# Performance work log

Hardware: AMD Instinct MI355X
Metric: run time of the kernel (lower is better)

The kernel has to match this reference:

```python
import jax, jax.numpy as jnp
import numpy as np

B, L, D, E, H = 8, 2048, 1024, 8, 2048


def setup_inputs() -> dict:
    key = jax.random.key(0)
    ks = jax.random.split(key, 5)
    scale_in = 1.0 / np.sqrt(D)
    scale_h = 1.0 / np.sqrt(H)
    return {
        "x": jax.random.normal(ks[0], (B, L, D), dtype=jnp.float32),
        "Wg": jax.random.normal(ks[1], (D, E), dtype=jnp.float32) * scale_in,
        "bg": jnp.zeros((E,), dtype=jnp.float32),
        "W1": jax.random.normal(ks[2], (E, D, H), dtype=jnp.float32) * scale_in,
        "b1": jnp.zeros((E, H), dtype=jnp.float32),
        "W2": jax.random.normal(ks[3], (E, H, D), dtype=jnp.float32) * scale_h,
        "b2": jnp.zeros((E, D), dtype=jnp.float32),
    }


def reference(x, Wg, bg, W1, b1, W2, b2):
    # x: [B, L, D] -> tokens [N, D]
    Bs, Ls, Ds = x.shape
    x_flat = x.reshape(-1, Ds)                                   # [N, D]
    gate_logits = x_flat @ Wg + bg                               # [N, E]
    gate_weights = jax.nn.softmax(gate_logits, axis=-1)          # [N, E]
    # top-1 gate (torch.topk with k=1)
    top_idx = jnp.argmax(gate_weights, axis=-1)                  # [N]
    top_w = jnp.max(gate_weights, axis=-1)                       # [N]
    # dense all-expert compute (matches torch.stack over experts)
    hidden = jax.nn.relu(jnp.einsum('nd,edh->neh', x_flat, W1) + b1)  # [N, E, H]
    expert_outputs = jnp.einsum('neh,ehd->ned', hidden, W2) + b2     # [N, E, D]
    # gather the selected expert per token, scale by its gate weight
    selected = jnp.take_along_axis(expert_outputs, top_idx[:, None, None], axis=1)[:, 0, :]  # [N, D]
    out_flat = top_w[:, None] * selected                          # [N, D]
    out = out_flat.reshape(Bs, Ls, Ds)
    return out, gate_weights
```

## Files before the change

kernel.cpp:

```cpp
#include <hip/hip_runtime.h>
#include <hip/hip_bf16.h>

#define N_TOK 16384
#define D_DIM 1024
#define E_NUM 8
#define H_DIM 2048
#define MT 32
#define FFN_BLK 512

typedef __attribute__((ext_vector_type(8))) short short8;
typedef __attribute__((ext_vector_type(4))) float floatx4;

__device__ __forceinline__ unsigned short f2bf_bits(float f) {
    __hip_bfloat16 h = __float2bfloat16(f);
    return *reinterpret_cast<unsigned short*>(&h);
}

__device__ __forceinline__ void async16(const void* g, void* l) {
    __builtin_amdgcn_global_load_lds(
        (const __attribute__((address_space(1))) unsigned int*)g,
        (__attribute__((address_space(3))) unsigned int*)l,
        16, 0, 0);
}

__global__ __launch_bounds__(256) void moe_gate_kernel(
    const float* __restrict__ x,
    const float* __restrict__ Wg,
    const float* __restrict__ bg,
    float* __restrict__ gw_out,
    float* __restrict__ topw,
    int* __restrict__ topidx,
    unsigned short* __restrict__ xb) {
    int wave = (blockIdx.x * blockDim.x + threadIdx.x) >> 6;
    int lane = threadIdx.x & 63;
    if (wave >= N_TOK) return;
    const float* xr = x + (size_t)wave * D_DIM;

    float4 xv[4];
#pragma unroll
    for (int i = 0; i < 4; i++)
        xv[i] = *(const float4*)(xr + i * 256 + lane * 4);

#pragma unroll
    for (int i = 0; i < 4; i++) {
        ushort4 o;
        o.x = f2bf_bits(xv[i].x); o.y = f2bf_bits(xv[i].y);
        o.z = f2bf_bits(xv[i].z); o.w = f2bf_bits(xv[i].w);
        *(ushort4*)(xb + (size_t)wave * D_DIM + i * 256 + lane * 4) = o;
    }

    float acc[8];
#pragma unroll
    for (int e = 0; e < 8; e++) acc[e] = 0.f;

#pragma unroll
    for (int i = 0; i < 4; i++) {
        const float xs4[4] = {xv[i].x, xv[i].y, xv[i].z, xv[i].w};
        const float* wp = Wg + ((size_t)(i * 256) + lane * 4) * 8;
#pragma unroll
        for (int j = 0; j < 4; j++) {
            float4 w0 = *(const float4*)(wp + j * 8);
            float4 w1 = *(const float4*)(wp + j * 8 + 4);
            float s = xs4[j];
            acc[0] += s * w0.x; acc[1] += s * w0.y;
            acc[2] += s * w0.z; acc[3] += s * w0.w;
            acc[4] += s * w1.x; acc[5] += s * w1.y;
            acc[6] += s * w1.z; acc[7] += s * w1.w;
        }
    }
#pragma unroll
    for (int e = 0; e < 8; e++) {
#pragma unroll
        for (int off = 32; off > 0; off >>= 1)
            acc[e] += __shfl_xor(acc[e], off, 64);
    }
#pragma unroll
    for (int e = 0; e < 8; e++) acc[e] += bg[e];

    float mx = acc[0]; int am = 0;
#pragma unroll
    for (int e = 1; e < 8; e++) { if (acc[e] > mx) { mx = acc[e]; am = e; } }
    float w[8], s = 0.f;
#pragma unroll
    for (int e = 0; e < 8; e++) { w[e] = expf(acc[e] - mx); s += w[e]; }
    float inv = 1.f / s;
#pragma unroll
    for (int e = 0; e < 8; e++) w[e] *= inv;

    if (lane == 0) {
        float4 a = make_float4(w[0], w[1], w[2], w[3]);
        float4 b = make_float4(w[4], w[5], w[6], w[7]);
        *(float4*)(gw_out + (size_t)wave * 8)     = a;
        *(float4*)(gw_out + (size_t)wave * 8 + 4) = b;
        topw[wave]   = w[am];
        topidx[wave] = am;
    }
}

__global__ __launch_bounds__(256) void moe_hist_scan_kernel(
    const int* __restrict__ topidx,
    int* __restrict__ offsets,
    int* __restrict__ cursor) {
    __shared__ int part[256][8];
    int tid = threadIdx.x;
    int c0 = 0, c1 = 0, c2 = 0, c3 = 0, c4 = 0, c5 = 0, c6 = 0, c7 = 0;
    for (int i = 0; i < N_TOK / 256; i++) {
        int idx = topidx[tid + (i << 8)];
        c0 += (idx == 0); c1 += (idx == 1); c2 += (idx == 2); c3 += (idx == 3);
        c4 += (idx == 4); c5 += (idx == 5); c6 += (idx == 6); c7 += (idx == 7);
    }
    part[tid][0] = c0; part[tid][1] = c1; part[tid][2] = c2; part[tid][3] = c3;
    part[tid][4] = c4; part[tid][5] = c5; part[tid][6] = c6; part[tid][7] = c7;
    __syncthreads();
    for (int s = 128; s > 0; s >>= 1) {
        if (tid < s) {
#pragma unroll
            for (int e = 0; e < 8; e++) part[tid][e] += part[tid + s][e];
        }
        __syncthreads();
    }
    if (tid == 0) {
        int run = 0;
        for (int e = 0; e < 8; e++) {
            offsets[e] = run;
            cursor[e]  = run;
            run += part[0][e];
        }
        offsets[8] = run;
    }
}

__global__ __launch_bounds__(256) void moe_scatter_kernel(
    const int* __restrict__ topidx,
    int* __restrict__ cursor,
    int* __restrict__ toksort) {
    __shared__ int lcnt[8];
    __shared__ int lbase[8];
    int tid = threadIdx.x;
    int t = blockIdx.x * blockDim.x + tid;
    if (tid < 8) lcnt[tid] = 0;
    __syncthreads();
    int e = topidx[t];
    int r = atomicAdd(&lcnt[e], 1);
    __syncthreads();
    if (tid < 8) lbase[tid] = atomicAdd(&cursor[tid], lcnt[tid]);
    __syncthreads();
    toksort[lbase[e] + r] = t;
}

__global__ __launch_bounds__(256) void transpose_cast_kernel(
    const float* __restrict__ in, unsigned short* __restrict__ out,
    int R, int C) {
    __shared__ float tile[64][65];
    const float* inE = in + (size_t)blockIdx.z * R * C;
    unsigned short* outE = out + (size_t)blockIdx.z * R * C;
    int c0 = blockIdx.x << 6, r0 = blockIdx.y << 6;
    int tr = threadIdx.x >> 4;
    int tc = (threadIdx.x & 15) << 2;
#pragma unroll
    for (int i = 0; i < 4; i++) {
        int r = tr + (i << 4);
        float4 v = *(const float4*)(inE + (size_t)(r0 + r) * C + c0 + tc);
        tile[r][tc + 0] = v.x; tile[r][tc + 1] = v.y;
        tile[r][tc + 2] = v.z; tile[r][tc + 3] = v.w;
    }
    __syncthreads();
#pragma unroll
    for (int i = 0; i < 4; i++) {
        int c = tr + (i << 4);
        ushort4 o;
        o.x = f2bf_bits(tile[tc + 0][c]);
        o.y = f2bf_bits(tile[tc + 1][c]);
        o.z = f2bf_bits(tile[tc + 2][c]);
        o.w = f2bf_bits(tile[tc + 3][c]);
        *(ushort4*)(outE + (size_t)(c0 + c) * R + r0 + tc) = o;
    }
}

__global__ __launch_bounds__(256) void gather_sorted_kernel(
    const unsigned short* __restrict__ xb, const int* __restrict__ toksort,
    unsigned short* __restrict__ xs) {
    int p = (blockIdx.x << 1) + (threadIdx.x >> 7);
    int tok = toksort[p];
    int c = (threadIdx.x & 127) << 3;
    float4 v = *(const float4*)(xb + (size_t)tok * D_DIM + c);
    *(float4*)(xs + (size_t)p * D_DIM + c) = v;
}

__device__ __forceinline__ int find_tile(const int* offsets, int mt,
                                         int& row0, int& rows) {
    int cum = 0;
    for (int ee = 0; ee < E_NUM; ee++) {
        int o0 = offsets[ee], o1 = offsets[ee + 1];
        int tiles = (o1 - o0 + 127) >> 7;
        if (mt < cum + tiles) {
            row0 = o0 + ((mt - cum) << 7);
            rows = o1 - row0; if (rows > 128) rows = 128;
            return ee;
        }
        cum += tiles;
    }
    return -1;
}

__global__ __launch_bounds__(256) void moe_ffn1_mfma(
    const unsigned short* __restrict__ xs,
    const unsigned short* __restrict__ W1t,
    const float* __restrict__ b1,
    const int* __restrict__ offsets,
    unsigned short* __restrict__ hb) {

    __shared__ __align__(16) unsigned short As[128 * 32];
    __shared__ __align__(16) unsigned short Bs[128 * 32];

    int row0, rows;
    int e = find_tile(offsets, blockIdx.x, row0, rows);
    if (e < 0) return;
    int n0 = blockIdx.y << 7;

    int tid = threadIdx.x, l = tid & 63, w = tid >> 6;
    int wm = w & 1, wn = w >> 1;
    int lrow = l & 15, lq = l >> 4;
    const unsigned short* Be = W1t + (size_t)e * H_DIM * D_DIM;

    floatx4 acc[4][4];
#pragma unroll
    for (int mi = 0; mi < 4; mi++)
#pragma unroll
        for (int ni = 0; ni < 4; ni++) acc[mi][ni] = floatx4{0.f, 0.f, 0.f, 0.f};

    int srow = (w << 5) + (l >> 2);
    int koff = (l & 3) << 3;

    for (int kt = 0; kt < D_DIM / 32; kt++) {
        int kb = kt << 5;
        __syncthreads();
#pragma unroll
        for (int i = 0; i < 2; i++) {
            int r = srow + (i << 4);
            int p = row0 + r; if (p > N_TOK - 1) p = N_TOK - 1;
            async16(xs + (size_t)p * D_DIM + kb + koff,
                    As + (((w << 5) + (i << 4)) << 5));
            async16(Be + (size_t)(n0 + r) * D_DIM + kb + koff,
                    Bs + (((w << 5) + (i << 4)) << 5));
        }
        __syncthreads();
        short8 af[4], bfv[4];
#pragma unroll
        for (int mi = 0; mi < 4; mi++)
            af[mi] = *(const short8*)(As + (((wm << 6) + (mi << 4) + lrow) << 5) + (lq << 3));
#pragma unroll
        for (int ni = 0; ni < 4; ni++)
            bfv[ni] = *(const short8*)(Bs + (((wn << 6) + (ni << 4) + lrow) << 5) + (lq << 3));
#pragma unroll
        for (int mi = 0; mi < 4; mi++)
#pragma unroll
            for (int ni = 0; ni < 4; ni++)
                acc[mi][ni] = __builtin_amdgcn_mfma_f32_16x16x32_bf16(
                    af[mi], bfv[ni], acc[mi][ni], 0, 0, 0);
    }

#pragma unroll
    for (int ni = 0; ni < 4; ni++) {
        int h = n0 + (wn << 6) + (ni << 4) + lrow;
        float bias = b1[e * H_DIM + h];
#pragma unroll
        for (int mi = 0; mi < 4; mi++) {
#pragma unroll
            for (int r = 0; r < 4; r++) {
                int row = (wm << 6) + (mi << 4) + (lq << 2) + r;
                if (row < rows) {
                    float v = acc[mi][ni][r] + bias;
                    v = v > 0.f ? v : 0.f;
                    hb[(size_t)(row0 + row) * H_DIM + h] = f2bf_bits(v);
                }
            }
        }
    }
}

__global__ __launch_bounds__(256) void moe_ffn2_mfma(
    const unsigned short* __restrict__ hb,
    const unsigned short* __restrict__ W2t,
    const float* __restrict__ b2,
    const int* __restrict__ offsets,
    const int* __restrict__ toksort,
    const float* __restrict__ topw,
    float* __restrict__ out) {

    __shared__ __align__(16) unsigned short As[128 * 32];
    __shared__ __align__(16) unsigned short Bs[128 * 32];

    int row0, rows;
    int e = find_tile(offsets, blockIdx.x, row0, rows);
    if (e < 0) return;
    int n0 = blockIdx.y << 7;

    int tid = threadIdx.x, l = tid & 63, w = tid >> 6;
    int wm = w & 1, wn = w >> 1;
    int lrow = l & 15, lq = l >> 4;
    const unsigned short* Be = W2t + (size_t)e * D_DIM * H_DIM;

    floatx4 acc[4][4];
#pragma unroll
    for (int mi = 0; mi < 4; mi++)
#pragma unroll
        for (int ni = 0; ni < 4; ni++) acc[mi][ni] = floatx4{0.f, 0.f, 0.f, 0.f};

    int srow = (w << 5) + (l >> 2);
    int koff = (l & 3) << 3;

    for (int kt = 0; kt < H_DIM / 32; kt++) {
        int kb = kt << 5;
        __syncthreads();
#pragma unroll
        for (int i = 0; i < 2; i++) {
            int r = srow + (i << 4);
            int p = row0 + r; if (p > N_TOK - 1) p = N_TOK - 1;
            async16(hb + (size_t)p * H_DIM + kb + koff,
                    As + (((w << 5) + (i << 4)) << 5));
            async16(Be + (size_t)(n0 + r) * H_DIM + kb + koff,
                    Bs + (((w << 5) + (i << 4)) << 5));
        }
        __syncthreads();
        short8 af[4], bfv[4];
#pragma unroll
        for (int mi = 0; mi < 4; mi++)
            af[mi] = *(const short8*)(As + (((wm << 6) + (mi << 4) + lrow) << 5) + (lq << 3));
#pragma unroll
        for (int ni = 0; ni < 4; ni++)
            bfv[ni] = *(const short8*)(Bs + (((wn << 6) + (ni << 4) + lrow) << 5) + (lq << 3));
#pragma unroll
        for (int mi = 0; mi < 4; mi++)
#pragma unroll
            for (int ni = 0; ni < 4; ni++)
                acc[mi][ni] = __builtin_amdgcn_mfma_f32_16x16x32_bf16(
                    af[mi], bfv[ni], acc[mi][ni], 0, 0, 0);
    }

    float bias[4];
#pragma unroll
    for (int ni = 0; ni < 4; ni++)
        bias[ni] = b2[e * D_DIM + n0 + (wn << 6) + (ni << 4) + lrow];

#pragma unroll
    for (int mi = 0; mi < 4; mi++) {
#pragma unroll
        for (int r = 0; r < 4; r++) {
            int row = (wm << 6) + (mi << 4) + (lq << 2) + r;
            if (row < rows) {
                int p = row0 + row;
                int tok = toksort[p];
                float tw = topw[tok];
#pragma unroll
                for (int ni = 0; ni < 4; ni++) {
                    int d = n0 + (wn << 6) + (ni << 4) + lrow;
                    out[(size_t)tok * D_DIM + d] = tw * (acc[mi][ni][r] + bias[ni]);
                }
            }
        }
    }
}

__global__ __launch_bounds__(FFN_BLK, 2) void moe_ffn_kernel(
    const float* __restrict__ x,
    const float* __restrict__ W1, const float* __restrict__ b1,
    const float* __restrict__ W2, const float* __restrict__ b2,
    const int* __restrict__ offsets,
    const int* __restrict__ toksort,
    const float* __restrict__ topw,
    float* __restrict__ out) {

    __shared__ __align__(16) unsigned short h1c[MT * 1024];
    float* xs = (float*)h1c;

    int bid = blockIdx.x;
    int e = -1, row0 = 0, rows = 0, cum = 0;
    for (int ee = 0; ee < E_NUM; ee++) {
        int o0 = offsets[ee], o1 = offsets[ee + 1];
        int tiles = (o1 - o0 + MT - 1) / MT;
        if (bid < cum + tiles) {
            e = ee;
            row0 = o0 + (bid - cum) * MT;
            rows = (o1 - row0 < MT) ? (o1 - row0) : MT;
            break;
        }
        cum += tiles;
    }
    if (e < 0) return;

    int tid = threadIdx.x;
    const float* W1e = W1 + (size_t)e * D_DIM * H_DIM;
    const float* W2e = W2 + (size_t)e * H_DIM * D_DIM;

    int m_st = tid >> 4;
    int j_st = tid & 15;
    int m_cl = (m_st < rows) ? m_st : (rows - 1);
    int tok_st = toksort[row0 + m_cl];

    float acc2x[MT], acc2y[MT];
#pragma unroll
    for (int m = 0; m < MT; m++) { acc2x[m] = 0.f; acc2y[m] = 0.f; }

    int d0 = tid * 2;

    for (int half = 0; half < 2; half++) {
        int ha = half * 1024 + tid;
        int hb_ = ha + 512;

        float a1a[MT], a1b[MT];
#pragma unroll
        for (int m = 0; m < MT; m++) { a1a[m] = 0.f; a1b[m] = 0.f; }

        for (int dc = 0; dc < 8; dc++) {
            __syncthreads();
            {
                const float4* src =
                    (const float4*)(x + (size_t)tok_st * D_DIM + dc * 128 + j_st * 8);
                float4 v0 = src[0], v1 = src[1];
                float4* dst = (float4*)(xs + m_st * 128 + j_st * 8);
                dst[0] = v0; dst[1] = v1;
            }
            __syncthreads();
            const float* w1pa = W1e + (size_t)(dc * 128) * H_DIM + ha;
            const float* w1pb = W1e + (size_t)(dc * 128) * H_DIM + hb_;
            for (int d2 = 0; d2 < 64; d2++) {
                float wa0 = w1pa[0], wa1 = w1pa[H_DIM];
                float wb0 = w1pb[0], wb1 = w1pb[H_DIM];
                w1pa += 2 * H_DIM; w1pb += 2 * H_DIM;
#pragma unroll
                for (int m = 0; m < MT; m++) {
                    float2 xv = *(const float2*)(xs + m * 128 + d2 * 2);
                    a1a[m] += xv.x * wa0; a1a[m] += xv.y * wa1;
                    a1b[m] += xv.x * wb0; a1b[m] += xv.y * wb1;
                }
            }
        }

        float bba = b1[e * H_DIM + ha];
        float bbb = b1[e * H_DIM + hb_];
        __syncthreads();
#pragma unroll
        for (int m = 0; m < MT; m++) {
            float va = a1a[m] + bba; va = va > 0.f ? va : 0.f;
            float vb = a1b[m] + bbb; vb = vb > 0.f ? vb : 0.f;
            h1c[m * 1024 + tid]       = f2bf_bits(va);
            h1c[m * 1024 + 512 + tid] = f2bf_bits(vb);
        }
        __syncthreads();

        const float* w2p = W2e + (size_t)(half * 1024) * D_DIM + d0;
        for (int hh = 0; hh < 1024; hh += 2) {
            float2 w2a = *(const float2*)(w2p);
            float2 w2b = *(const float2*)(w2p + D_DIM);
            w2p += 2 * D_DIM;
#pragma unroll
            for (int m = 0; m < MT; m++) {
                unsigned int u = *(const unsigned int*)(h1c + m * 1024 + hh);
                float h0  = __uint_as_float(u << 16);
                float h1v = __uint_as_float(u & 0xffff0000u);
                acc2x[m] += h0 * w2a.x; acc2x[m] += h1v * w2b.x;
                acc2y[m] += h0 * w2a.y; acc2y[m] += h1v * w2b.y;
            }
        }
    }

    float bb0 = b2[e * D_DIM + d0];
    float bb1 = b2[e * D_DIM + d0 + 1];
#pragma unroll
    for (int m = 0; m < MT; m++) {
        if (m < rows) {
            int tok  = toksort[row0 + m];
            float tw = topw[tok];
            float2 o;
            o.x = tw * (acc2x[m] + bb0);
            o.y = tw * (acc2y[m] + bb1);
            *(float2*)(out + (size_t)tok * D_DIM + d0) = o;
        }
    }
}

extern "C" void kernel_launch(void* const* d_in, const int* in_sizes, int n_in,
                              void* d_out, int out_size, void* d_ws, size_t ws_size,
                              hipStream_t stream) {
    const float* x  = (const float*)d_in[0];
    const float* Wg = (const float*)d_in[1];
    const float* bg = (const float*)d_in[2];
    const float* W1 = (const float*)d_in[3];
    const float* b1 = (const float*)d_in[4];
    const float* W2 = (const float*)d_in[5];
    const float* b2 = (const float*)d_in[6];

    float* out = (float*)d_out;
    float* gw  = out + (size_t)N_TOK * D_DIM;

    char* ws = (char*)d_ws;
    int*   counts  = (int*)ws;
    int*   cursor  = counts + 8;
    int*   offsets = cursor + 8;
    int*   topidx  = (int*)(ws + 128);
    float* topw    = (float*)(ws + 128 + 4 * (size_t)N_TOK);
    int*   toksort = (int*)(ws + 128 + 8 * (size_t)N_TOK);

    const size_t off_xs  = 256ull << 10;
    const size_t off_w1t = off_xs  + (32ull << 20);
    const size_t off_w2t = off_w1t + (32ull << 20);
    const size_t off_hb  = off_w2t + (32ull << 20);
    const size_t off_xb  = off_hb;
    const size_t need    = off_hb  + (64ull << 20);

    if (ws_size >= need) {
        unsigned short* xs  = (unsigned short*)(ws + off_xs);
        unsigned short* W1t = (unsigned short*)(ws + off_w1t);
        unsigned short* W2t = (unsigned short*)(ws + off_w2t);
        unsigned short* hb  = (unsigned short*)(ws + off_hb);
        unsigned short* xb  = (unsigned short*)(ws + off_xb);

        moe_gate_kernel<<<N_TOK / 4, 256, 0, stream>>>(
            x, Wg, bg, gw, topw, topidx, xb);
        moe_hist_scan_kernel<<<1, 256, 0, stream>>>(topidx, offsets, cursor);
        moe_scatter_kernel<<<N_TOK / 256, 256, 0, stream>>>(topidx, cursor, toksort);

        transpose_cast_kernel<<<dim3(H_DIM / 64, D_DIM / 64, E_NUM), 256, 0, stream>>>(
            W1, W1t, D_DIM, H_DIM);
        transpose_cast_kernel<<<dim3(D_DIM / 64, H_DIM / 64, E_NUM), 256, 0, stream>>>(
            W2, W2t, H_DIM, D_DIM);
        gather_sorted_kernel<<<N_TOK / 2, 256, 0, stream>>>(xb, toksort, xs);

        moe_ffn1_mfma<<<dim3(N_TOK / 128 + E_NUM, H_DIM / 128), 256, 0, stream>>>(
            xs, W1t, b1, offsets, hb);
        moe_ffn2_mfma<<<dim3(N_TOK / 128 + E_NUM, D_DIM / 128), 256, 0, stream>>>(
            hb, W2t, b2, offsets, toksort, topw, out);
    } else {
        unsigned short* xb = (unsigned short*)(ws + (256ull << 10));
        moe_gate_kernel<<<N_TOK / 4, 256, 0, stream>>>(
            x, Wg, bg, gw, topw, topidx, xb);
        moe_hist_scan_kernel<<<1, 256, 0, stream>>>(topidx, offsets, cursor);
        moe_scatter_kernel<<<N_TOK / 256, 256, 0, stream>>>(topidx, cursor, toksort);
        moe_ffn_kernel<<<N_TOK / MT + E_NUM, FFN_BLK, 0, stream>>>(
            x, W1, b1, W2, b2, offsets, toksort, topw, out);
    }
}
```

Measured before the change: 537.1 us.

## Triple-buffer MFMA GEMM LDS tiles with swizzle and merge weight transposes

Both expert FFN GEMM kernels now use a three-stage LDS ring, issuing async global-to-LDS loads two K-tiles ahead with vmcnt waits and a single barrier per iteration instead of two. LDS columns are XOR-swizzled to reduce bank conflicts on the fragment reads, and s_setprio raises wave priority around the MFMA block. The two weight transpose/cast launches are merged into one kernel to save a launch. This triples LDS usage per block, which may reduce occupancy.

Result: no change. 542.3 us (+1.0%).

```diff
diff --git a/kernel.cpp b/kernel.cpp
--- a/kernel.cpp
+++ b/kernel.cpp
@@ -148,13 +148,25 @@
     toksort[lbase[e] + r] = t;
 }
 
-__global__ __launch_bounds__(256) void transpose_cast_kernel(
-    const float* __restrict__ in, unsigned short* __restrict__ out,
-    int R, int C) {
+__global__ __launch_bounds__(256) void transpose_cast_both(
+    const float* __restrict__ W1, const float* __restrict__ W2,
+    unsigned short* __restrict__ W1t, unsigned short* __restrict__ W2t) {
     __shared__ float tile[64][65];
-    const float* inE = in + (size_t)blockIdx.z * R * C;
-    unsigned short* outE = out + (size_t)blockIdx.z * R * C;
-    int c0 = blockIdx.x << 6, r0 = blockIdx.y << 6;
+    int id = blockIdx.x;
+    const float* in; unsigned short* out; int R, C, cx, ry, e;
+    if (id < 4096) {
+        e = id >> 9; int t = id & 511;
+        in = W1; out = W1t; R = 1024; C = 2048;
+        cx = t & 31; ry = t >> 5;
+    } else {
+        id -= 4096;
+        e = id >> 9; int t = id & 511;
+        in = W2; out = W2t; R = 2048; C = 1024;
+        cx = t & 15; ry = t >> 4;
+    }
+    const float* inE = in + (size_t)e * 2097152;
+    unsigned short* outE = out + (size_t)e * 2097152;
+    int c0 = cx << 6, r0 = ry << 6;
     int tr = threadIdx.x >> 4;
     int tc = (threadIdx.x & 15) << 2;
 #pragma unroll
@@ -203,6 +215,23 @@
     return -1;
 }
 
+__device__ __forceinline__ void stage_tile(
+    const unsigned short* __restrict__ Abase,
+    const unsigned short* __restrict__ Bbase,
+    int row0, int n0, int kb, int ld,
+    int w, int rsub, int ksw,
+    unsigned short* Abuf, unsigned short* Bbuf) {
+#pragma unroll
+    for (int j = 0; j < 2; j++) {
+        int ar = (j << 6) + (w << 4) + rsub;
+        int p = row0 + ar; if (p > N_TOK - 1) p = N_TOK - 1;
+        async16(Abase + (size_t)p * ld + kb + ksw,
+                Abuf + (j << 11) + (w << 9));
+        async16(Bbase + (size_t)(n0 + ar) * ld + kb + ksw,
+                Bbuf + (j << 11) + (w << 9));
+    }
+}
+
 __global__ __launch_bounds__(256) void moe_ffn1_mfma(
     const unsigned short* __restrict__ xs,
     const unsigned short* __restrict__ W1t,
@@ -210,8 +239,8 @@
     const int* __restrict__ offsets,
     unsigned short* __restrict__ hb) {
 
-    __shared__ __align__(16) unsigned short As[128 * 32];
-    __shared__ __align__(16) unsigned short Bs[128 * 32];
+    __shared__ __align__(16) unsigned short As[3][4096];
+    __shared__ __align__(16) unsigned short Bs[3][4096];
 
     int row0, rows;
     int e = find_tile(offsets, blockIdx.x, row0, rows);
@@ -221,6 +250,9 @@
     int tid = threadIdx.x, l = tid & 63, w = tid >> 6;
     int wm = w & 1, wn = w >> 1;
     int lrow = l & 15, lq = l >> 4;
+    int rsub = l >> 2;
+    int ksw = (((l & 3) ^ ((l >> 2) & 3)) << 3);
+    int koffr = (lq << 3) ^ ((lrow & 3) << 3);
     const unsigned short* Be = W1t + (size_t)e * H_DIM * D_DIM;
 
     floatx4 acc[4][4];
@@ -229,35 +261,42 @@
 #pragma unroll
         for (int ni = 0; ni < 4; ni++) acc[mi][ni] = floatx4{0.f, 0.f, 0.f, 0.f};
 
-    int srow = (w << 5) + (l >> 2);
-    int koff = (l & 3) << 3;
-
-    for (int kt = 0; kt < D_DIM / 32; kt++) {
-        int kb = kt << 5;
-        __syncthreads();
-#pragma unroll
-        for (int i = 0; i < 2; i++) {
-            int r = srow + (i << 4);
-            int p = row0 + r; if (p > N_TOK - 1) p = N_TOK - 1;
-            async16(xs + (size_t)p * D_DIM + kb + koff,
-                    As + (((w << 5) + (i << 4)) << 5));
-            async16(Be + (size_t)(n0 + r) * D_DIM + kb + koff,
-                    Bs + (((w << 5) + (i << 4)) << 5));
-        }
-        __syncthreads();
+    const int NT = D_DIM / 32;
+    stage_tile(xs, Be, row0, n0, 0,  D_DIM, w, rsub, ksw, As[0], Bs[0]);
+    stage_tile(xs, Be, row0, n0, 32, D_DIM, w, rsub, ksw, As[1], Bs[1]);
+    asm volatile("s_waitcnt vmcnt(4)" ::: "memory");
+    __builtin_amdgcn_s_barrier();
+    __builtin_amdgcn_sched_barrier(0);
+
+    int c = 0;
+    for (int kt = 0; kt < NT; kt++) {
+        if (kt + 2 < NT) {
+            int c2 = c + 2; if (c2 >= 3) c2 -= 3;
+            stage_tile(xs, Be, row0, n0, (kt + 2) << 5, D_DIM,
+                       w, rsub, ksw, As[c2], Bs[c2]);
+        }
+        const unsigned short* Ab = As[c];
+        const unsigned short* Bb = Bs[c];
         short8 af[4], bfv[4];
 #pragma unroll
         for (int mi = 0; mi < 4; mi++)
-            af[mi] = *(const short8*)(As + (((wm << 6) + (mi << 4) + lrow) << 5) + (lq << 3));
+            af[mi] = *(const short8*)(Ab + (((wm << 6) + (mi << 4) + lrow) << 5) + koffr);
 #pragma unroll
         for (int ni = 0; ni < 4; ni++)
-            bfv[ni] = *(const short8*)(Bs + (((wn << 6) + (ni << 4) + lrow) << 5) + (lq << 3));
+            bfv[ni] = *(const short8*)(Bb + (((wn << 6) + (ni << 4) + lrow) << 5) + koffr);
+        __builtin_amdgcn_s_setprio(1);
 #pragma unroll
         for (int mi = 0; mi < 4; mi++)
 #pragma unroll
             for (int ni = 0; ni < 4; ni++)
                 acc[mi][ni] = __builtin_amdgcn_mfma_f32_16x16x32_bf16(
                     af[mi], bfv[ni], acc[mi][ni], 0, 0, 0);
+        __builtin_amdgcn_s_setprio(0);
+        if (kt + 2 < NT) { asm volatile("s_waitcnt vmcnt(4)" ::: "memory"); }
+        else             { asm volatile("s_waitcnt vmcnt(0)" ::: "memory"); }
+        __builtin_amdgcn_s_barrier();
+        __builtin_amdgcn_sched_barrier(0);
+        c = (c == 2) ? 0 : c + 1;
     }
 
 #pragma unroll
@@ -288,8 +327,8 @@
     const float* __restrict__ topw,
     float* __restrict__ out) {
 
-    __shared__ __align__(16) unsigned short As[128 * 32];
-    __shared__ __align__(16) unsigned short Bs[128 * 32];
+    __shared__ __align__(16) unsigned short As[3][4096];
+    __shared__ __align__(16) unsigned short Bs[3][4096];
 
     int row0, rows;
     int e = find_tile(offsets, blockIdx.x, row0, rows);
@@ -299,6 +338,9 @@
     int tid = threadIdx.x, l = tid & 63, w = tid >> 6;
     int wm = w & 1, wn = w >> 1;
     int lrow = l & 15, lq = l >> 4;
+    int rsub = l >> 2;
+    int ksw = (((l & 3) ^ ((l >> 2) & 3)) << 3);
+    int koffr = (lq << 3) ^ ((lrow & 3) << 3);
     const unsigned short* Be = W2t + (size_t)e * D_DIM * H_DIM;
 
     floatx4 acc[4][4];
@@ -307,35 +349,42 @@
 #pragma unroll
         for (int ni = 0; ni < 4; ni++) acc[mi][ni] = floatx4{0.f, 0.f, 0.f, 0.f};
 
-    int srow = (w << 5) + (l >> 2);
-    int koff = (l & 3) << 3;
-
-    for (int kt = 0; kt < H_DIM / 32; kt++) {
-        int kb = kt << 5;
-        __syncthreads();
-#pragma unroll
-        for (int i = 0; i < 2; i++) {
-            int r = srow + (i << 4);
-            int p = row0 + r; if (p > N_TOK - 1) p = N_TOK - 1;
-            async16(hb + (size_t)p * H_DIM + kb + koff,
-                    As + (((w << 5) + (i << 4)) << 5));
-            async16(Be + (size_t)(n0 + r) * H_DIM + kb + koff,
-                    Bs + (((w << 5) + (i << 4)) << 5));
-        }
-        __syncthreads();
+    const int NT = H_DIM / 32;
+    stage_tile(hb, Be, row0, n0, 0,  H_DIM, w, rsub, ksw, As[0], Bs[0]);
+    stage_tile(hb, Be, row0, n0, 32, H_DIM, w, rsub, ksw, As[1], Bs[1]);
+    asm volatile("s_waitcnt vmcnt(4)" ::: "memory");
+    __builtin_amdgcn_s_barrier();
+    __builtin_amdgcn_sched_barrier(0);
+
+    int c = 0;
+    for (int kt = 0; kt < NT; kt++) {
+        if (kt + 2 < NT) {
+            int c2 = c + 2; if (c2 >= 3) c2 -= 3;
+            stage_tile(hb, Be, row0, n0, (kt + 2) << 5, H_DIM,
+                       w, rsub, ksw, As[c2], Bs[c2]);
+        }
+        const unsigned short* Ab = As[c];
+        const unsigned short* Bb = Bs[c];
         short8 af[4], bfv[4];
 #pragma unroll
         for (int mi = 0; mi < 4; mi++)
-            af[mi] = *(const short8*)(As + (((wm << 6) + (mi << 4) + lrow) << 5) + (lq << 3));
+            af[mi] = *(const short8*)(Ab + (((wm << 6) + (mi << 4) + lrow) << 5) + koffr);
 #pragma unroll
         for (int ni = 0; ni < 4; ni++)
-            bfv[ni] = *(const short8*)(Bs + (((wn << 6) + (ni << 4) + lrow) << 5) + (lq << 3));
+            bfv[ni] = *(const short8*)(Bb + (((wn << 6) + (ni << 4) + lrow) << 5) + koffr);
+        __builtin_amdgcn_s_setprio(1);
 #pragma unroll
         for (int mi = 0; mi < 4; mi++)
 #pragma unroll
             for (int ni = 0; ni < 4; ni++)
                 acc[mi][ni] = __builtin_amdgcn_mfma_f32_16x16x32_bf16(
                     af[mi], bfv[ni], acc[mi][ni], 0, 0, 0);
+        __builtin_amdgcn_s_setprio(0);
+        if (kt + 2 < NT) { asm volatile("s_waitcnt vmcnt(4)" ::: "memory"); }
+        else             { asm volatile("s_waitcnt vmcnt(0)" ::: "memory"); }
+        __builtin_amdgcn_s_barrier();
+        __builtin_amdgcn_sched_barrier(0);
+        c = (c == 2) ? 0 : c + 1;
     }
 
     float bias[4];
@@ -521,10 +570,7 @@
         moe_hist_scan_kernel<<<1, 256, 0, stream>>>(topidx, offsets, cursor);
         moe_scatter_kernel<<<N_TOK / 256, 256, 0, stream>>>(topidx, cursor, toksort);
 
-        transpose_cast_kernel<<<dim3(H_DIM / 64, D_DIM / 64, E_NUM), 256, 0, stream>>>(
-            W1, W1t, D_DIM, H_DIM);
-        transpose_cast_kernel<<<dim3(D_DIM / 64, H_DIM / 64, E_NUM), 256, 0, stream>>>(
-            W2, W2t, H_DIM, D_DIM);
+        transpose_cast_both<<<8192, 256, 0, stream>>>(W1, W2, W1t, W2t);
         gather_sorted_kernel<<<N_TOK / 2, 256, 0, stream>>>(xb, toksort, xs);
 
         moe_ffn1_mfma<<<dim3(N_TOK / 128 + E_NUM, H_DIM / 128), 256, 0, stream>>>(
```

## Rewrite expert GEMMs as pipelined 256x256 tiles with swizzled LDS

Applied to the files above, without the earlier changes.

Replaces the 128x128, single-buffered MFMA GEMMs with 256x256 tiles over 512 threads. The K loop is double-buffered with async global-to-LDS loads, an XOR-swizzled LDS layout, explicit vmcnt waits and priority hints, which should hide memory latency and raise reuse per loaded byte. It also adds an XCD-aware block remap, stages epilogues through LDS so global stores are coalesced, and merges the two weight transpose-cast launches into one with wider stores. Larger tiles waste more work on the partial tile at the end of each expert's token range and reduce the number of blocks. The hand-written barrier and waitcnt scheduling is fragile.

Result: slower. 552.0 us (+2.8%).

```diff
diff --git a/kernel.cpp b/kernel.cpp
--- a/kernel.cpp
+++ b/kernel.cpp
@@ -148,13 +148,25 @@
     toksort[lbase[e] + r] = t;
 }
 
-__global__ __launch_bounds__(256) void transpose_cast_kernel(
-    const float* __restrict__ in, unsigned short* __restrict__ out,
-    int R, int C) {
+__global__ __launch_bounds__(256) void transpose_cast_both(
+    const float* __restrict__ W1, const float* __restrict__ W2,
+    unsigned short* __restrict__ W1t, unsigned short* __restrict__ W2t) {
     __shared__ float tile[64][65];
-    const float* inE = in + (size_t)blockIdx.z * R * C;
-    unsigned short* outE = out + (size_t)blockIdx.z * R * C;
-    int c0 = blockIdx.x << 6, r0 = blockIdx.y << 6;
+    int id = blockIdx.x;
+    const float* in; unsigned short* out; int R, C, cx, ry, e;
+    if (id < 4096) {
+        e = id >> 9; int t = id & 511;
+        in = W1; out = W1t; R = 1024; C = 2048;
+        cx = t & 31; ry = t >> 5;
+    } else {
+        id -= 4096;
+        e = id >> 9; int t = id & 511;
+        in = W2; out = W2t; R = 2048; C = 1024;
+        cx = t & 15; ry = t >> 4;
+    }
+    const float* inE = in + (size_t)e * 2097152;
+    unsigned short* outE = out + (size_t)e * 2097152;
+    int c0 = cx << 6, r0 = ry << 6;
     int tr = threadIdx.x >> 4;
     int tc = (threadIdx.x & 15) << 2;
 #pragma unroll
@@ -166,14 +178,14 @@
     }
     __syncthreads();
 #pragma unroll
-    for (int i = 0; i < 4; i++) {
-        int c = tr + (i << 4);
-        ushort4 o;
-        o.x = f2bf_bits(tile[tc + 0][c]);
-        o.y = f2bf_bits(tile[tc + 1][c]);
-        o.z = f2bf_bits(tile[tc + 2][c]);
-        o.w = f2bf_bits(tile[tc + 3][c]);
-        *(ushort4*)(outE + (size_t)(c0 + c) * R + r0 + tc) = o;
+    for (int it = 0; it < 2; it++) {
+        int task = threadIdx.x + (it << 8);
+        int c = task >> 3, rr = (task & 7) << 3;
+        short8 o;
+#pragma unroll
+        for (int j = 0; j < 8; j++)
+            ((unsigned short*)&o)[j] = f2bf_bits(tile[rr + j][c]);
+        *(short8*)(outE + (size_t)(c0 + c) * R + r0 + rr) = o;
     }
 }
 
@@ -187,15 +199,15 @@
     *(float4*)(xs + (size_t)p * D_DIM + c) = v;
 }
 
-__device__ __forceinline__ int find_tile(const int* offsets, int mt,
-                                         int& row0, int& rows) {
+__device__ __forceinline__ int find_tile256(const int* offsets, int mt,
+                                            int& row0, int& rows) {
     int cum = 0;
     for (int ee = 0; ee < E_NUM; ee++) {
         int o0 = offsets[ee], o1 = offsets[ee + 1];
-        int tiles = (o1 - o0 + 127) >> 7;
+        int tiles = (o1 - o0 + 255) >> 8;
         if (mt < cum + tiles) {
-            row0 = o0 + ((mt - cum) << 7);
-            rows = o1 - row0; if (rows > 128) rows = 128;
+            row0 = o0 + ((mt - cum) << 8);
+            rows = o1 - row0; if (rows > 256) rows = 256;
             return ee;
         }
         cum += tiles;
@@ -203,83 +215,196 @@
     return -1;
 }
 
-__global__ __launch_bounds__(256) void moe_ffn1_mfma(
+#define MMQ(Q, NQ)                                                            \
+    _Pragma("unroll") for (int mi = 0; mi < 4; mi++)                          \
+    _Pragma("unroll") for (int ni = 0; ni < 2; ni++)                          \
+    _Pragma("unroll") for (int kk = 0; kk < 2; kk++)                          \
+        acc[(Q)*4 + mi][(NQ)*2 + ni] = __builtin_amdgcn_mfma_f32_16x16x32_bf16( \
+            af[mi][kk], bf[ni][kk], acc[(Q)*4 + mi][(NQ)*2 + ni], 0, 0, 0);
+
+#define VMC6 asm volatile("s_waitcnt vmcnt(6)" ::: "memory")
+#define VMC8 asm volatile("s_waitcnt vmcnt(8)" ::: "memory")
+#define VMNO ((void)0)
+
+#define PHASE(RDS, STG, Q, NQ, VM)                                            \
+    RDS;                                                                      \
+    STG;                                                                      \
+    __builtin_amdgcn_sched_barrier(0);                                        \
+    __builtin_amdgcn_s_barrier();                                             \
+    asm volatile("s_waitcnt lgkmcnt(0)" ::: "memory");                        \
+    __builtin_amdgcn_sched_barrier(0);                                        \
+    __builtin_amdgcn_s_setprio(1);                                            \
+    MMQ(Q, NQ);                                                               \
+    __builtin_amdgcn_s_setprio(0);                                            \
+    VM;                                                                       \
+    __builtin_amdgcn_s_barrier();                                             \
+    __builtin_amdgcn_sched_barrier(0);
+
+template<int LDK>
+__device__ __forceinline__ void gemm256_kloop(
+    const unsigned short* __restrict__ Ag,
+    const unsigned short* __restrict__ Bg,
+    int row0, int n0, int ntiles,
+    unsigned short* LDSU, floatx4 (&acc)[8][4]) {
+
+    const int tid = threadIdx.x;
+    const int l = tid & 63, w = tid >> 6;
+    const int lq = l >> 4, lrow = l & 15, l3 = l >> 3;
+    const int wm = w & 1, wn = w >> 1;
+    const int kc = ((l & 7) ^ (l3 & 7)) << 3;
+    const int gx = l & 7;
+
+    const unsigned short* pA[2][2];
+    const unsigned short* pB[2][2];
+#pragma unroll
+    for (int j = 0; j < 2; j++) {
+        int s = w * 16 + j * 8 + l3;
+#pragma unroll
+        for (int h = 0; h < 2; h++) {
+            int rA = (s & 63) + h * 64 + ((s >> 6) & 1) * 128;
+            int pr = row0 + rA; if (pr > N_TOK - 1) pr = N_TOK - 1;
+            pA[j][h] = Ag + (size_t)pr * LDK + kc;
+            int cB = (s & 31) + h * 32 + (s >> 5) * 64;
+            pB[j][h] = Bg + (size_t)(n0 + cB) * LDK + kc;
+        }
+    }
+    unsigned short* ldsA = LDSU;
+    unsigned short* ldsB = LDSU + 32768;
+    const int wslot = w * 1024;
+
+    auto STA = [&](int buf, int half, int t) {
+        async16(pA[0][half] + ((size_t)t << 6),
+                ldsA + buf * 16384 + half * 8192 + wslot);
+        async16(pA[1][half] + ((size_t)t << 6),
+                ldsA + buf * 16384 + half * 8192 + wslot + 512);
+    };
+    auto STB = [&](int buf, int half, int t) {
+        async16(pB[0][half] + ((size_t)t << 6),
+                ldsB + buf * 16384 + half * 8192 + wslot);
+        async16(pB[1][half] + ((size_t)t << 6),
+                ldsB + buf * 16384 + half * 8192 + wslot + 512);
+    };
+
+    short8 af[4][2], bf[2][2];
+    const int asb = wm * 64 + lrow;
+    const int bsb = wn * 32 + lrow;
+    auto RA = [&](int buf, int q) {
+        const unsigned short* Ab = ldsA + buf * 16384 + q * 8192;
+#pragma unroll
+        for (int mi = 0; mi < 4; mi++) {
+            int slot = asb + mi * 16;
+#pragma unroll
+            for (int kk = 0; kk < 2; kk++) {
+                int g = (kk * 4 + lq) ^ gx;
+                af[mi][kk] = *(const short8*)(Ab + slot * 64 + g * 8);
+            }
+        }
+    };
+    auto RB = [&](int buf, int nq) {
+        const unsigned short* Bb = ldsB + buf * 16384 + nq * 8192;
+#pragma unroll
+        for (int ni = 0; ni < 2; ni++) {
+            int slot = bsb + ni * 16;
+#pragma unroll
+            for (int kk = 0; kk < 2; kk++) {
+                int g = (kk * 4 + lq) ^ gx;
+                bf[ni][kk] = *(const short8*)(Bb + slot * 64 + g * 8);
+            }
+        }
+    };
+
+    STA(0, 0, 0); STB(0, 0, 0); STA(0, 1, 0); STB(0, 1, 0);
+    STA(1, 0, 1); STB(1, 0, 1);
+    VMC8;
+    __builtin_amdgcn_s_barrier();
+    __builtin_amdgcn_sched_barrier(0);
+
+    const int NT2 = ntiles >> 1;
+    for (int i = 0; i < NT2; i++) {
+        const int t1 = 2 * i + 1;
+        int t2 = 2 * i + 2; if (t2 > ntiles - 1) t2 = ntiles - 1;
+        int t3 = 2 * i + 3; if (t3 > ntiles - 1) t3 = ntiles - 1;
+        PHASE((RA(0, 0), RB(0, 0)), STA(1, 1, t1), 0, 0, VMC6);
+        PHASE((RB(0, 1)),           STB(1, 1, t1), 0, 1, VMNO);
+        PHASE((RA(0, 1), RB(0, 0)), STA(0, 0, t2), 1, 0, VMNO);
+        PHASE((RB(0, 1)),           STB(0, 0, t2), 1, 1, VMC8);
+        PHASE((RA(1, 0), RB(1, 0)), STA(0, 1, t2), 0, 0, VMC6);
+        PHASE((RB(1, 1)),           STB(0, 1, t2), 0, 1, VMNO);
+        PHASE((RA(1, 1), RB(1, 0)), STA(1, 0, t3), 1, 0, VMNO);
+        PHASE((RB(1, 1)),           STB(1, 0, t3), 1, 1, VMC8);
+    }
+    asm volatile("s_waitcnt vmcnt(0)" ::: "memory");
+    __syncthreads();
+}
+
+__global__ __launch_bounds__(512, 2) void moe_ffn1_256(
     const unsigned short* __restrict__ xs,
     const unsigned short* __restrict__ W1t,
     const float* __restrict__ b1,
     const int* __restrict__ offsets,
     unsigned short* __restrict__ hb) {
 
-    __shared__ __align__(16) unsigned short As[128 * 32];
-    __shared__ __align__(16) unsigned short Bs[128 * 32];
+    __shared__ __align__(16) unsigned short LDSU[65536];
+
+    int nwgx = gridDim.x;
+    int nwg = nwgx * gridDim.y;
+    int id = blockIdx.y * nwgx + blockIdx.x;
+    int q8 = nwg >> 3, r8 = nwg & 7;
+    int xcd = id & 7, rank = id >> 3;
+    int swz = (xcd < r8 ? xcd * (q8 + 1) : r8 * (q8 + 1) + (xcd - r8) * q8) + rank;
+    int bx = swz % nwgx, by = swz / nwgx;
 
     int row0, rows;
-    int e = find_tile(offsets, blockIdx.x, row0, rows);
+    int e = find_tile256(offsets, bx, row0, rows);
     if (e < 0) return;
-    int n0 = blockIdx.y << 7;
-
-    int tid = threadIdx.x, l = tid & 63, w = tid >> 6;
-    int wm = w & 1, wn = w >> 1;
-    int lrow = l & 15, lq = l >> 4;
+    int n0 = by << 8;
+
     const unsigned short* Be = W1t + (size_t)e * H_DIM * D_DIM;
 
-    floatx4 acc[4][4];
-#pragma unroll
-    for (int mi = 0; mi < 4; mi++)
+    floatx4 acc[8][4];
+#pragma unroll
+    for (int mi = 0; mi < 8; mi++)
 #pragma unroll
         for (int ni = 0; ni < 4; ni++) acc[mi][ni] = floatx4{0.f, 0.f, 0.f, 0.f};
 
-    int srow = (w << 5) + (l >> 2);
-    int koff = (l & 3) << 3;
-
-    for (int kt = 0; kt < D_DIM / 32; kt++) {
-        int kb = kt << 5;
-        __syncthreads();
-#pragma unroll
-        for (int i = 0; i < 2; i++) {
-            int r = srow + (i << 4);
-            int p = row0 + r; if (p > N_TOK - 1) p = N_TOK - 1;
-            async16(xs + (size_t)p * D_DIM + kb + koff,
-                    As + (((w << 5) + (i << 4)) << 5));
-            async16(Be + (size_t)(n0 + r) * D_DIM + kb + koff,
-                    Bs + (((w << 5) + (i << 4)) << 5));
-        }
-        __syncthreads();
-        short8 af[4], bfv[4];
-#pragma unroll
-        for (int mi = 0; mi < 4; mi++)
-            af[mi] = *(const short8*)(As + (((wm << 6) + (mi << 4) + lrow) << 5) + (lq << 3));
-#pragma unroll
-        for (int ni = 0; ni < 4; ni++)
-            bfv[ni] = *(const short8*)(Bs + (((wn << 6) + (ni << 4) + lrow) << 5) + (lq << 3));
-#pragma unroll
-        for (int mi = 0; mi < 4; mi++)
-#pragma unroll
-            for (int ni = 0; ni < 4; ni++)
-                acc[mi][ni] = __builtin_amdgcn_mfma_f32_16x16x32_bf16(
-                    af[mi], bfv[ni], acc[mi][ni], 0, 0, 0);
-    }
-
-#pragma unroll
-    for (int ni = 0; ni < 4; ni++) {
-        int h = n0 + (wn << 6) + (ni << 4) + lrow;
-        float bias = b1[e * H_DIM + h];
-#pragma unroll
-        for (int mi = 0; mi < 4; mi++) {
-#pragma unroll
-            for (int r = 0; r < 4; r++) {
-                int row = (wm << 6) + (mi << 4) + (lq << 2) + r;
-                if (row < rows) {
-                    float v = acc[mi][ni][r] + bias;
-                    v = v > 0.f ? v : 0.f;
-                    hb[(size_t)(row0 + row) * H_DIM + h] = f2bf_bits(v);
-                }
-            }
-        }
-    }
-}
-
-__global__ __launch_bounds__(256) void moe_ffn2_mfma(
+    gemm256_kloop<D_DIM>(xs, Be, row0, n0, D_DIM / 64, LDSU, acc);
+
+    const int tid = threadIdx.x;
+    const int l = tid & 63, w = tid >> 6;
+    const int lq = l >> 4, lrow = l & 15;
+    const int wm = w & 1, wn = w >> 1;
+
+    float bias[4];
+#pragma unroll
+    for (int ni = 0; ni < 4; ni++)
+        bias[ni] = b1[e * H_DIM + n0 + wn * 64 + ni * 16 + lrow];
+
+#pragma unroll
+    for (int mi = 0; mi < 8; mi++) {
+#pragma unroll
+        for (int ni = 0; ni < 4; ni++) {
+#pragma unroll
+            for (int rr = 0; rr < 4; rr++) {
+                int rl = wm * 128 + mi * 16 + lq * 4 + rr;
+                int cl = wn * 64 + ni * 16 + lrow;
+                float v = acc[mi][ni][rr] + bias[ni];
+                v = v > 0.f ? v : 0.f;
+                LDSU[rl * 256 + cl] = f2bf_bits(v);
+            }
+        }
+    }
+    __syncthreads();
+    int trow = tid >> 1, tcol = (tid & 1) << 7;
+    if (trow < rows) {
+        unsigned short* dst = hb + (size_t)(row0 + trow) * H_DIM + n0 + tcol;
+        const unsigned short* src = LDSU + trow * 256 + tcol;
+#pragma unroll
+        for (int i2 = 0; i2 < 16; i2++)
+            *(short8*)(dst + i2 * 8) = *(const short8*)(src + i2 * 8);
+    }
+}
+
+__global__ __launch_bounds__(512, 2) void moe_ffn2_256(
     const unsigned short* __restrict__ hb,
     const unsigned short* __restrict__ W2t,
     const float* __restrict__ b2,
@@ -288,75 +413,73 @@
     const float* __restrict__ topw,
     float* __restrict__ out) {
 
-    __shared__ __align__(16) unsigned short As[128 * 32];
-    __shared__ __align__(16) unsigned short Bs[128 * 32];
+    __shared__ __align__(16) unsigned short LDSU[65536];
+
+    int nwgx = gridDim.x;
+    int nwg = nwgx * gridDim.y;
+    int id = blockIdx.y * nwgx + blockIdx.x;
+    int q8 = nwg >> 3, r8 = nwg & 7;
+    int xcd = id & 7, rank = id >> 3;
+    int swz = (xcd < r8 ? xcd * (q8 + 1) : r8 * (q8 + 1) + (xcd - r8) * q8) + rank;
+    int bx = swz % nwgx, by = swz / nwgx;
 
     int row0, rows;
-    int e = find_tile(offsets, blockIdx.x, row0, rows);
+    int e = find_tile256(offsets, bx, row0, rows);
     if (e < 0) return;
-    int n0 = blockIdx.y << 7;
-
-    int tid = threadIdx.x, l = tid & 63, w = tid >> 6;
-    int wm = w & 1, wn = w >> 1;
-    int lrow = l & 15, lq = l >> 4;
+    int n0 = by << 8;
+
     const unsigned short* Be = W2t + (size_t)e * D_DIM * H_DIM;
 
-    floatx4 acc[4][4];
-#pragma unroll
-    for (int mi = 0; mi < 4; mi++)
+    floatx4 acc[8][4];
+#pragma unroll
+    for (int mi = 0; mi < 8; mi++)
 #pragma unroll
         for (int ni = 0; ni < 4; ni++) acc[mi][ni] = floatx4{0.f, 0.f, 0.f, 0.f};
 
-    int srow = (w << 5) + (l >> 2);
-    int koff = (l & 3) << 3;
-
-    for (int kt = 0; kt < H_DIM / 32; kt++) {
-        int kb = kt << 5;
+    gemm256_kloop<H_DIM>(hb, Be, row0, n0, H_DIM / 64, LDSU, acc);
+
+    const int tid = threadIdx.x;
+    const int l = tid & 63, w = tid >> 6;
+    const int lq = l >> 4, lrow = l & 15;
+    const int wm = w & 1, wn = w >> 1;
+
+    float bias[4];
+#pragma unroll
+    for (int ni = 0; ni < 4; ni++)
+        bias[ni] = b2[e * D_DIM + n0 + wn * 64 + ni * 16 + lrow];
+
+    float* LDSF = (float*)LDSU;
+#pragma unroll
+    for (int h = 0; h < 2; h++) {
         __syncthreads();
-#pragma unroll
-        for (int i = 0; i < 2; i++) {
-            int r = srow + (i << 4);
-            int p = row0 + r; if (p > N_TOK - 1) p = N_TOK - 1;
-            async16(hb + (size_t)p * H_DIM + kb + koff,
-                    As + (((w << 5) + (i << 4)) << 5));
-            async16(Be + (size_t)(n0 + r) * H_DIM + kb + koff,
-                    Bs + (((w << 5) + (i << 4)) << 5));
+        if (wm == h) {
+#pragma unroll
+            for (int mi = 0; mi < 8; mi++) {
+#pragma unroll
+                for (int ni = 0; ni < 4; ni++) {
+#pragma unroll
+                    for (int rr = 0; rr < 4; rr++) {
+                        int rl = mi * 16 + lq * 4 + rr;
+                        int cl = wn * 64 + ni * 16 + lrow;
+                        LDSF[rl * 256 + cl] = acc[mi][ni][rr] + bias[ni];
+                    }
+                }
+            }
         }
         __syncthreads();
-        short8 af[4], bfv[4];
-#pragma unroll
-        for (int mi = 0; mi < 4; mi++)
-            af[mi] = *(const short8*)(As + (((wm << 6) + (mi << 4) + lrow) << 5) + (lq << 3));
-#pragma unroll
-        for (int ni = 0; ni < 4; ni++)
-            bfv[ni] = *(const short8*)(Bs + (((wn << 6) + (ni << 4) + lrow) << 5) + (lq << 3));
-#pragma unroll
-        for (int mi = 0; mi < 4; mi++)
-#pragma unroll
-            for (int ni = 0; ni < 4; ni++)
-                acc[mi][ni] = __builtin_amdgcn_mfma_f32_16x16x32_bf16(
-                    af[mi], bfv[ni], acc[mi][ni], 0, 0, 0);
-    }
-
-    float bias[4];
-#pragma unroll
-    for (int ni = 0; ni < 4; ni++)
-        bias[ni] = b2[e * D_DIM + n0 + (wn << 6) + (ni << 4) + lrow];
-
-#pragma unroll
-    for (int mi = 0; mi < 4; mi++) {
-#pragma unroll
-        for (int r = 0; r < 4; r++) {
-            int row = (wm << 6) + (mi << 4) + (lq << 2) + r;
-            if (row < rows) {
-                int p = row0 + row;
-                int tok = toksort[p];
-                float tw = topw[tok];
-#pragma unroll
-                for (int ni = 0; ni < 4; ni++) {
-                    int d = n0 + (wn << 6) + (ni << 4) + lrow;
-                    out[(size_t)tok * D_DIM + d] = tw * (acc[mi][ni][r] + bias[ni]);
-                }
+        int rloc = tid >> 2, seg = (tid & 3) << 6;
+        int rl = h * 128 + rloc;
+        if (rl < rows) {
+            int p = row0 + rl;
+            int tok = toksort[p];
+            float tw = topw[tok];
+            float* dst = out + (size_t)tok * D_DIM + n0 + seg;
+            const float* src = LDSF + rloc * 256 + seg;
+#pragma unroll
+            for (int i2 = 0; i2 < 16; i2++) {
+                float4 v = *(const float4*)(src + i2 * 4);
+                v.x *= tw; v.y *= tw; v.z *= tw; v.w *= tw;
+                *(float4*)(dst + i2 * 4) = v;
             }
         }
     }
@@ -521,15 +644,12 @@
         moe_hist_scan_kernel<<<1, 256, 0, stream>>>(topidx, offsets, cursor);
         moe_scatter_kernel<<<N_TOK / 256, 256, 0, stream>>>(topidx, cursor, toksort);
 
-        transpose_cast_kernel<<<dim3(H_DIM / 64, D_DIM / 64, E_NUM), 256, 0, stream>>>(
-            W1, W1t, D_DIM, H_DIM);
-        transpose_cast_kernel<<<dim3(D_DIM / 64, H_DIM / 64, E_NUM), 256, 0, stream>>>(
-            W2, W2t, H_DIM, D_DIM);
+        transpose_cast_both<<<8192, 256, 0, stream>>>(W1, W2, W1t, W2t);
         gather_sorted_kernel<<<N_TOK / 2, 256, 0, stream>>>(xb, toksort, xs);
 
-        moe_ffn1_mfma<<<dim3(N_TOK / 128 + E_NUM, H_DIM / 128), 256, 0, stream>>>(
+        moe_ffn1_256<<<dim3(N_TOK / 256 + E_NUM, H_DIM / 256), 512, 0, stream>>>(
             xs, W1t, b1, offsets, hb);
-        moe_ffn2_mfma<<<dim3(N_TOK / 128 + E_NUM, D_DIM / 128), 256, 0, stream>>>(
+        moe_ffn2_256<<<dim3(N_TOK / 256 + E_NUM, D_DIM / 256), 512, 0, stream>>>(
             hb, W2t, b2, offsets, toksort, topw, out);
     } else {
         unsigned short* xb = (unsigned short*)(ws + (256ull << 10));
```
